# Kernel optimization log

Hardware: AMD Instinct MI355X
Metric: run time of the kernel (lower is better)

Reference implementation:

```python
import jax, jax.numpy as jnp
import numpy as np
from jax import lax

EPS = 1e-5
NUM_GROUPS = 32
OFFSET_SCALE = 1.0
K = 3            # deformable conv kernel size
KK = K * K
DWK = 7          # depthwise kernel size for offset predictor


def group_norm(x, gamma, beta, num_groups=NUM_GROUPS):
    B, C, H, W = x.shape
    xg = x.reshape(B, num_groups, C // num_groups, H, W)
    m = xg.mean(axis=(2, 3, 4), keepdims=True)
    v = xg.var(axis=(2, 3, 4), keepdims=True)
    xn = ((xg - m) * lax.rsqrt(v + EPS)).reshape(B, C, H, W)
    return xn * gamma[None, :, None, None] + beta[None, :, None, None]


def bilinear_gather(x, py, px):
    # x: [B,C,H,W]; py, px: [B,KK,H,W] absolute sample coords -> [B,C,KK,H,W]
    B, C, H, W = x.shape
    y0 = jnp.floor(py)
    x0 = jnp.floor(px)
    wy1 = py - y0
    wx1 = px - x0
    wy0 = 1.0 - wy1
    wx0 = 1.0 - wx1
    xf = x.reshape(B, C, H * W)

    def gather(yi, xi):
        valid = (yi >= 0) & (yi <= H - 1) & (xi >= 0) & (xi <= W - 1)
        yc = jnp.clip(yi, 0, H - 1).astype(jnp.int32)
        xc = jnp.clip(xi, 0, W - 1).astype(jnp.int32)
        idx = (yc * W + xc).reshape(B, -1)                      # [B, KK*H*W]
        g = jax.vmap(lambda a, i: a[:, i])(xf, idx)             # [B, C, KK*H*W]
        g = g.reshape(B, C, KK, H, W)
        return g * valid.astype(x.dtype)[:, None]

    out = (gather(y0, x0) * (wy0 * wx0)[:, None]
           + gather(y0, x0 + 1.0) * (wy0 * wx1)[:, None]
           + gather(y0 + 1.0, x0) * (wy1 * wx0)[:, None]
           + gather(y0 + 1.0, x0 + 1.0) * (wy1 * wx1)[:, None])
    return out


def deform_conv(x, dw, pw, pwb, w, b):
    # x: [B,C,H,W]; dw: [C,1,DWK,DWK] depthwise; pw: [2*KK,C,1,1]; w: [O,C,K,K]
    B, C, H, W = x.shape
    dn = ('NCHW', 'OIHW', 'NCHW')
    f = lax.conv_general_dilated(x, dw, (1, 1), 'SAME',
                                 feature_group_count=C, dimension_numbers=dn)
    off = lax.conv_general_dilated(f, pw, (1, 1), 'SAME', dimension_numbers=dn)
    off = (off + pwb[None, :, None, None]) * OFFSET_SCALE       # [B,2*KK,H,W]
    off = off.reshape(B, KK, 2, H, W)
    ks = jnp.arange(K, dtype=x.dtype) - (K - 1) / 2             # [-1,0,1]
    ky = jnp.repeat(ks, K)                                      # [KK]
    kx = jnp.tile(ks, K)
    yy, xx = jnp.meshgrid(jnp.arange(H, dtype=x.dtype),
                          jnp.arange(W, dtype=x.dtype), indexing='ij')
    py = yy[None, None] + ky[None, :, None, None] + off[:, :, 0]  # [B,KK,H,W]
    px = xx[None, None] + kx[None, :, None, None] + off[:, :, 1]
    sampled = bilinear_gather(x, py, px)                        # [B,C,KK,H,W]
    O = w.shape[0]
    out = jnp.einsum('bckhw,ock->bohw', sampled, w.reshape(O, C, KK))
    return out + b[None, :, None, None]


def setup_inputs() -> dict:
    key = jax.random.key(0)
    ks = jax.random.split(key, 10)
    B, C, H, W = 4, 256, 64, 64
    O = C
    x = jax.random.normal(ks[0], (B, C, H, W), dtype=jnp.float32)

    def conv_w(k, shape, fan_in):
        return jax.random.normal(k, shape, dtype=jnp.float32) / np.sqrt(fan_in)

    inp = {
        'x': x,
        'gn1_g': jnp.ones((C,), jnp.float32), 'gn1_b': jnp.zeros((C,), jnp.float32),
        'dw1': conv_w(ks[1], (C, 1, DWK, DWK), DWK * DWK),
        'pw1': jax.random.normal(ks[2], (2 * KK, C, 1, 1), jnp.float32) * 0.01,
        'pwb1': jnp.zeros((2 * KK,), jnp.float32),
        'w1': conv_w(ks[3], (O, C, K, K), C * KK),
        'b1': jnp.zeros((O,), jnp.float32),
        'gn2_g': jnp.ones((O,), jnp.float32), 'gn2_b': jnp.zeros((O,), jnp.float32),
        'dw2': conv_w(ks[4], (O, 1, DWK, DWK), DWK * DWK),
        'pw2': jax.random.normal(ks[5], (2 * KK, O, 1, 1), jnp.float32) * 0.01,
        'pwb2': jnp.zeros((2 * KK,), jnp.float32),
        'w2': conv_w(ks[6], (O, O, K, K), O * KK),
        'b2': jnp.zeros((O,), jnp.float32),
    }
    return inp


def reference(x, gn1_g, gn1_b, dw1, pw1, pwb1, w1, b1,
              gn2_g, gn2_b, dw2, pw2, pwb2, w2, b2):
    h = jax.nn.relu(group_norm(x, gn1_g, gn1_b))
    h = deform_conv(h, dw1, pw1, pwb1, w1, b1)
    h = jax.nn.relu(group_norm(h, gn2_g, gn2_b))
    # Dropout / DropPath are identity in eval mode
    h = deform_conv(h, dw2, pw2, pwb2, w2, b2)
    return h + x  # shortcut is Identity (in_channels == out_channels)
```

## Files before the change

### kernel.cpp

```cpp
#include <hip/hip_runtime.h>

#define B_    4
#define C_    256
#define H_    64
#define W_    64
#define HW_   4096
#define NG_   32
#define CPG_  8
#define KK_   9
#define NOFF_ 18

typedef __attribute__((ext_vector_type(8))) short short8;
typedef __attribute__((ext_vector_type(4))) short short4v;
typedef __attribute__((ext_vector_type(4))) float floatx4;
typedef __attribute__((ext_vector_type(16))) float floatx16;

static __device__ __forceinline__ short f2bf(float f) {
    union { float f; unsigned u; } v; v.f = f;
    unsigned r = v.u + 0x7fff + ((v.u >> 16) & 1);
    return (short)(r >> 16);
}
static __device__ __forceinline__ float bf2f(short s) {
    union { unsigned u; float f; } v;
    v.u = ((unsigned)(unsigned short)s) << 16;
    return v.f;
}
static __device__ __forceinline__ unsigned pkbf(float lo, float hi) {
    unsigned r;
    asm("v_cvt_pk_bf16_f32 %0, %1, %2" : "=v"(r) : "v"(lo), "v"(hi));
    return r;
}

__global__ __launch_bounds__(1024) void gn_relu_f32_kernel(
    const float* __restrict__ in, const float* __restrict__ gamma,
    const float* __restrict__ beta, short* __restrict__ outb)
{
    __shared__ float cache[32768];
    __shared__ float red[32];
    __shared__ float sh_rs, sh_m;
    int b = blockIdx.x >> 5;
    int g = blockIdx.x & 31;
    const int N = CPG_ * HW_;
    size_t base = ((size_t)(b * C_ + g * CPG_)) * HW_;
    const float4* in4 = (const float4*)(in + base);
    int t = threadIdx.x;

    float s = 0.f, ss = 0.f;
    for (int i = t; i < N / 4; i += 1024) {
        float4 v = in4[i];
        *(float4*)&cache[i * 4] = v;
        s  += v.x + v.y + v.z + v.w;
        ss += v.x * v.x + v.y * v.y + v.z * v.z + v.w * v.w;
    }
    #pragma unroll
    for (int off = 32; off > 0; off >>= 1) {
        s  += __shfl_down(s, off, 64);
        ss += __shfl_down(ss, off, 64);
    }
    int wid = t >> 6;
    if ((t & 63) == 0) { red[wid] = s; red[16 + wid] = ss; }
    __syncthreads();
    if (t == 0) {
        float S = 0.f, SS = 0.f;
        #pragma unroll
        for (int i = 0; i < 16; ++i) { S += red[i]; SS += red[16 + i]; }
        float m = S / (float)N;
        float var = SS / (float)N - m * m;
        sh_rs = rsqrtf(var + 1e-5f);
        sh_m = m;
    }
    __syncthreads();
    float rs = sh_rs, m = sh_m;
    short4v* out4 = (short4v*)(outb + base);
    for (int i = t; i < N / 4; i += 1024) {
        int ch = g * CPG_ + (i >> 10);
        float ga = gamma[ch] * rs;
        float be = beta[ch] - m * ga;
        float4 v = *(const float4*)&cache[i * 4];
        short4v o;
        o.x = f2bf(fmaxf(fmaf(v.x, ga, be), 0.f));
        o.y = f2bf(fmaxf(fmaf(v.y, ga, be), 0.f));
        o.z = f2bf(fmaxf(fmaf(v.z, ga, be), 0.f));
        o.w = f2bf(fmaxf(fmaf(v.w, ga, be), 0.f));
        out4[i] = o;
    }
}

__global__ __launch_bounds__(1024) void gn_apply_bf16_kernel(
    const short* __restrict__ in, const float* __restrict__ gstats,
    const float* __restrict__ gamma, const float* __restrict__ beta,
    short* __restrict__ outb)
{
    int blk = blockIdx.x;
    int b = blk >> 7, g = (blk >> 2) & 31, qq = blk & 3;
    const float Ninv = 1.f / (float)(CPG_ * HW_);
    int sidx = b * 32 + g;
    float m   = gstats[sidx] * Ninv;
    float var = gstats[128 + sidx] * Ninv - m * m;
    float rs  = rsqrtf(var + 1e-5f);
    size_t base = ((size_t)(b * C_ + g * CPG_)) * HW_;
    const short4v* in4 = (const short4v*)(in + base);
    short4v* out4 = (short4v*)(outb + base);
    int t = threadIdx.x;
    int i0 = qq * 2048;
    for (int i = i0 + t; i < i0 + 2048; i += 1024) {
        int ch = g * CPG_ + (i >> 10);
        float ga = gamma[ch] * rs;
        float be = beta[ch] - m * ga;
        short4v sv = in4[i];
        short4v o;
        o.x = f2bf(fmaxf(fmaf(bf2f(sv.x), ga, be), 0.f));
        o.y = f2bf(fmaxf(fmaf(bf2f(sv.y), ga, be), 0.f));
        o.z = f2bf(fmaxf(fmaf(bf2f(sv.z), ga, be), 0.f));
        o.w = f2bf(fmaxf(fmaf(bf2f(sv.w), ga, be), 0.f));
        out4[i] = o;
    }
}

__global__ __launch_bounds__(256) void dw7t_tr_kernel(
    const short* __restrict__ in,
    const float* __restrict__ dwk,
    short* __restrict__ fdwt,
    short* __restrict__ ht)
{
    __shared__ __align__(16) char smem[78112];
    int t = threadIdx.x;
    int blk = blockIdx.x;
    if (blk < 256) {
        short (*tile)[38][72] = (short(*)[38][72])smem;
        float (*wk8)[49]      = (float(*)[49])(smem + 43776);
        short (*outs)[2048]   = (short(*)[2048])(smem + 45344);
        int b = blk >> 6, o8 = (blk >> 1) & 31, rh = blk & 1;
        int c0 = o8 * 8;
        unsigned* tz = (unsigned*)smem;
        for (int i = t; i < 10944; i += 256) tz[i] = 0u;
        for (int i = t; i < 392; i += 256)
            wk8[i / 49][i % 49] = dwk[(c0 + i / 49) * 49 + (i % 49)];
        __syncthreads();
        for (int ch = 0; ch < 8; ++ch) {
            const short* src = in + ((size_t)(b * C_ + c0 + ch)) * HW_;
            for (int i = t; i < 608; i += 256) {
                int rr = i >> 4, xq = i & 15;
                int ry = rh * 32 + rr - 3;
                if (ry >= 0 && ry < 64) {
                    short4v v = *(const short4v*)(src + ry * 64 + xq * 4);
                    *(short4v*)&tile[ch][rr][4 + xq * 4] = v;
                }
            }
        }
        __syncthreads();
        for (int it = 0; it < 16; ++it) {
            int q = it * 256 + t;
            int ch = q >> 9, y = (q >> 4) & 31, x0 = (q & 15) << 2;
            float a0 = 0.f, a1 = 0.f, a2 = 0.f, a3 = 0.f;
            const float* wr0 = wk8[ch];
            #pragma unroll
            for (int dy = 0; dy < 7; ++dy) {
                const short* trw = &tile[ch][y + dy][x0];
                short4v s0 = *(const short4v*)trw;
                short4v s1 = *(const short4v*)(trw + 4);
                short4v s2 = *(const short4v*)(trw + 8);
                float r[12] = {bf2f(s0.x), bf2f(s0.y), bf2f(s0.z), bf2f(s0.w),
                               bf2f(s1.x), bf2f(s1.y), bf2f(s1.z), bf2f(s1.w),
                               bf2f(s2.x), bf2f(s2.y), bf2f(s2.z), bf2f(s2.w)};
                const float* wr = wr0 + dy * 7;
                #pragma unroll
                for (int dx = 0; dx < 7; ++dx) {
                    float wv = wr[dx];
                    a0 = fmaf(r[dx + 1], wv, a0);
                    a1 = fmaf(r[dx + 2], wv, a1);
                    a2 = fmaf(r[dx + 3], wv, a2);
                    a3 = fmaf(r[dx + 4], wv, a3);
                }
            }
            short4v o;
            o.x = f2bf(a0); o.y = f2bf(a1); o.z = f2bf(a2); o.w = f2bf(a3);
            *(short4v*)&outs[ch][y * 64 + x0] = o;
        }
        __syncthreads();
        for (int it = 0; it < 8; ++it) {
            int p = it * 256 + t;
            short8 v;
            #pragma unroll
            for (int ch = 0; ch < 8; ++ch) v[ch] = outs[ch][p];
            *(short8*)(fdwt + (((size_t)(b * 64 + rh * 32 + (p >> 6)) * 32 + o8) * 64
                               + (p & 63)) * 8) = v;
        }
    } else {
        unsigned* ltile = (unsigned*)smem;
        int q0 = blk - 256;
        int q = ((q0 & 7) << 5) | (q0 >> 3);
        int b = q >> 6;
        int px0 = (q & 63) * 64;
        const short* sb = in + (size_t)b * C_ * HW_;
        int pq4 = t & 15, cphi = t >> 4;
        #pragma unroll
        for (int i = 0; i < 8; ++i) {
            int cp = i * 16 + cphi;
            const short* r0 = sb + (size_t)(2 * cp) * HW_ + px0 + pq4 * 4;
            short4v lo = *(const short4v*)r0;
            short4v hi = *(const short4v*)(r0 + HW_);
            #pragma unroll
            for (int j = 0; j < 4; ++j) {
                int pl = pq4 * 4 + j;
                unsigned wrd = (unsigned)(unsigned short)lo[j]
                             | ((unsigned)(unsigned short)hi[j] << 16);
                ltile[pl * 132 + (cp ^ ((pl & 7) << 2))] = wrd;
            }
        }
        __syncthreads();
        int co = t & 31, ph2 = t >> 5;
        #pragma unroll
        for (int r = 0; r < 8; ++r) {
            int pl = r * 8 + ph2;
            uint4 v = *(const uint4*)&ltile[pl * 132 + ((co * 4) ^ ((pl & 7) << 2))];
            *(uint4*)(ht + ((size_t)b * HW_ + px0 + pl) * C_ + co * 8) = v;
        }
    }
}

__global__ __launch_bounds__(256) void wpack_all_kernel(
    const float* __restrict__ w1, const float* __restrict__ w2,
    const float* __restrict__ pw1, const float* __restrict__ pw2,
    short* __restrict__ wp1, short* __restrict__ wp2,
    short* __restrict__ ppk1, short* __restrict__ ppk2)
{
    int blk = blockIdx.x;
    if (blk < 4608) {
        const float* w = (blk < 2304) ? w1 : w2;
        short* wp = (blk < 2304) ? wp1 : wp2;
        int src = (blk % 2304) * 256 + threadIdx.x;
        float v = w[src];
        int o = src / (C_ * KK_);
        int r = src - o * (C_ * KK_);
        int c = r / KK_;
        int g = r - c * KK_;
        int ot   = o >> 5;
        int lane = (o & 31) | (((c >> 3) & 1) << 5);
        int j    = c & 7;
        int slab = g * 16 + (c >> 4);
        wp[(slab << 12) | (ot << 9) | (lane << 3) | j] = f2bf(v);
    } else {
        int q = blk - 4608;
        const float* pw = (q < 32) ? pw1 : pw2;
        short* ppk = (q < 32) ? ppk1 : ppk2;
        int idx = (q & 31) * 256 + threadIdx.x;
        int j = idx & 7, lane = (idx >> 3) & 63;
        int ot = (idx >> 9) & 1, sl = idx >> 10;
        int o = ot * 16 + (lane & 15);
        int k = sl * 32 + (lane >> 4) * 8 + j;
        ppk[idx] = (o < NOFF_) ? f2bf(pw[o * C_ + k]) : (short)0;
    }
}

__global__ __launch_bounds__(1024, 4) void deform_fused_kernel(
    const short* __restrict__ ht,   const short* __restrict__ fdw,
    const short* __restrict__ ppk,  const float* __restrict__ pwb,
    const short* __restrict__ wp,   const float* __restrict__ bias,
    const float* __restrict__ resid, float* __restrict__ outf,
    short* __restrict__ outb,       float* __restrict__ gstats)
{
    int lb = ((blockIdx.x & 7) << 5) | (blockIdx.x >> 3);
    int b = lb >> 6;
    int row = lb & 63;
    __shared__ int   i00[576], i01[576], i10[576], i11[576];
    __shared__ float c00[576], c01[576], c10[576], c11[576];
    __shared__ __align__(16) short sbuf[2][2][8192];
    __shared__ float stat_lds[16][8];
    float* off_lds = (float*)&sbuf[0][0][0];
    int t = threadIdx.x;
    int wv = t >> 6, lane = t & 63;
    int pq = lane >> 4, pr = lane & 15;
    int l31 = lane & 31, hi = lane >> 5;

    if (wv < 8) {
        int ot = wv & 1, ptw = wv >> 1;
        int px = ptw * 16 + pr;
        const short8* fdw8 = (const short8*)fdw;
        size_t fbase = ((size_t)(b * 64 + row)) * 32;
        const short8* ap = (const short8*)ppk;
        floatx4 pacc = (floatx4){0.f, 0.f, 0.f, 0.f};
        #pragma unroll
        for (int sl = 0; sl < 8; ++sl) {
            short8 af = ap[(sl * 2 + ot) * 64 + lane];
            short8 bf = fdw8[(fbase + sl * 4 + pq) * 64 + px];
            pacc = __builtin_amdgcn_mfma_f32_16x16x32_bf16(af, bf, pacc, 0, 0, 0);
        }
        #pragma unroll
        for (int r = 0; r < 4; ++r) {
            int o = ot * 16 + pq * 4 + r;
            if (o < NOFF_) off_lds[o * 64 + px] = pacc[r] + pwb[o];
        }
    }
    __syncthreads();

    if (t < 576) {
        int e = t;
        int k = e >> 6, p = e & 63;
        float offy = off_lds[(2 * k) * 64 + p];
        float offx = off_lds[(2 * k + 1) * 64 + p];
        float py = (float)row + (float)(k / 3 - 1) + offy;
        float px = (float)p   + (float)(k % 3 - 1) + offx;
        float y0f = floorf(py), x0f = floorf(px);
        float wy1 = py - y0f, wx1 = px - x0f;
        float wy0 = 1.f - wy1, wx0 = 1.f - wx1;
        float y1f = y0f + 1.f, x1f = x0f + 1.f;
        bool vy0 = (y0f >= 0.f) && (y0f <= 63.f);
        bool vy1 = (y1f >= 0.f) && (y1f <= 63.f);
        bool vx0 = (x0f >= 0.f) && (x0f <= 63.f);
        bool vx1 = (x1f >= 0.f) && (x1f <= 63.f);
        int iy0 = (int)fminf(fmaxf(y0f, 0.f), 63.f);
        int iy1 = (int)fminf(fmaxf(y1f, 0.f), 63.f);
        int ix0 = (int)fminf(fmaxf(x0f, 0.f), 63.f);
        int ix1 = (int)fminf(fmaxf(x1f, 0.f), 63.f);
        i00[e] = iy0 * 64 + ix0; i01[e] = iy0 * 64 + ix1;
        i10[e] = iy1 * 64 + ix0; i11[e] = iy1 * 64 + ix1;
        c00[e] = (vy0 && vx0) ? wy0 * wx0 : 0.f;
        c01[e] = (vy0 && vx1) ? wy0 * wx1 : 0.f;
        c10[e] = (vy1 && vx0) ? wy1 * wx0 : 0.f;
        c11[e] = (vy1 && vx1) ? wy1 * wx1 : 0.f;
    }
    __syncthreads();

    int c8a = t & 7;
    int pan = (t >> 3) & 1;
    int spx = t >> 4;
    const short* hb0 = ht + ((size_t)b * HW_) * C_ + pan * 128 + c8a * 8;
    const short* hb1 = hb0 + 64;
    int slotA = (c8a ^ (spx & 15)) * 8;
    int slotB = ((c8a + 8) ^ (spx & 15)) * 8;
    int srow = spx * 128;

    short8 ra[4], rb[4];
    auto prefetch = [&](int g) {
        int e = g * 64 + spx;
        int a00 = i00[e], a01 = i01[e], a10 = i10[e], a11 = i11[e];
        ra[0] = *(const short8*)(hb0 + (size_t)a00 * C_);
        ra[1] = *(const short8*)(hb0 + (size_t)a01 * C_);
        ra[2] = *(const short8*)(hb0 + (size_t)a10 * C_);
        ra[3] = *(const short8*)(hb0 + (size_t)a11 * C_);
        rb[0] = *(const short8*)(hb1 + (size_t)a00 * C_);
        rb[1] = *(const short8*)(hb1 + (size_t)a01 * C_);
        rb[2] = *(const short8*)(hb1 + (size_t)a10 * C_);
        rb[3] = *(const short8*)(hb1 + (size_t)a11 * C_);
    };
    auto stage_write = [&](int g, int bi) {
        int e = g * 64 + spx;
        float w00 = c00[e], w01 = c01[e], w10 = c10[e], w11 = c11[e];
        uint4 va, vb;
        float f0, f1;
        #define BLEND(R, J) (w00 * bf2f(R[0][J]) + w01 * bf2f(R[1][J]) \
                           + w10 * bf2f(R[2][J]) + w11 * bf2f(R[3][J]))
        f0 = BLEND(ra, 0); f1 = BLEND(ra, 1); va.x = pkbf(f0, f1);
        f0 = BLEND(ra, 2); f1 = BLEND(ra, 3); va.y = pkbf(f0, f1);
        f0 = BLEND(ra, 4); f1 = BLEND(ra, 5); va.z = pkbf(f0, f1);
        f0 = BLEND(ra, 6); f1 = BLEND(ra, 7); va.w = pkbf(f0, f1);
        f0 = BLEND(rb, 0); f1 = BLEND(rb, 1); vb.x = pkbf(f0, f1);
        f0 = BLEND(rb, 2); f1 = BLEND(rb, 3); vb.y = pkbf(f0, f1);
        f0 = BLEND(rb, 4); f1 = BLEND(rb, 5); vb.z = pkbf(f0, f1);
        f0 = BLEND(rb, 6); f1 = BLEND(rb, 7); vb.w = pkbf(f0, f1);
        #undef BLEND
        short* sp = &sbuf[bi][pan][srow];
        *(uint4*)&sp[slotA] = va;
        *(uint4*)&sp[slotB] = vb;
    };

    int pairId = wv & 7;
    int half = wv >> 3;

    floatx16 acc[2];
    #pragma unroll
    for (int i = 0; i < 16; ++i) { acc[0][i] = 0.f; acc[1][i] = 0.f; }

    prefetch(0);
    stage_write(0, 0);
    prefetch(1);
    __syncthreads();

    const short8* wp8 = (const short8*)wp;
    int msk = l31 & 15;

    for (int g = 0; g < 9; ++g) {
        const short* sb = &sbuf[g & 1][half][0];
        #pragma unroll
        for (int q4 = 0; q4 < 2; ++q4) {
            short8 af[4];
            #pragma unroll
            for (int qq = 0; qq < 4; ++qq)
                af[qq] = wp8[(size_t)(((g * 16 + half * 8 + q4 * 4 + qq) * 8 + pairId) * 64 + lane)];
            #pragma unroll
            for (int qq = 0; qq < 4; ++qq) {
                int ksl = q4 * 4 + qq;
                int so = ((((ksl << 1) | hi) ^ msk) << 3);
                short8 b0 = *(const short8*)&sb[l31 * 128 + so];
                short8 b1 = *(const short8*)&sb[(32 + l31) * 128 + so];
                acc[0] = __builtin_amdgcn_mfma_f32_32x32x16_bf16(af[qq], b0, acc[0], 0, 0, 0);
                acc[1] = __builtin_amdgcn_mfma_f32_32x32x16_bf16(af[qq], b1, acc[1], 0, 0, 0);
            }
        }
        if (g + 1 < 9) {
            stage_write(g + 1, (g + 1) & 1);
            if (g + 2 < 9) prefetch(g + 2);
        }
        __syncthreads();
    }

    float* xch = (float*)&sbuf[0][0][0];
    int wreg = (pairId * 2 + half) * 1024;
    floatx16 aw = half ? acc[0] : acc[1];
    floatx4* xq = (floatx4*)xch;
    #pragma unroll
    for (int j = 0; j < 4; ++j) {
        floatx4 v = {aw[j * 4 + 0], aw[j * 4 + 1], aw[j * 4 + 2], aw[j * 4 + 3]};
        xq[(wreg >> 2) + j * 64 + lane] = v;
    }
    __syncthreads();
    int rreg = (pairId * 2 + (half ^ 1)) * 1024;
    floatx16 ac = half ? acc[1] : acc[0];
    #pragma unroll
    for (int j = 0; j < 4; ++j) {
        floatx4 v = xq[(rreg >> 2) + j * 64 + lane];
        ac[j * 4 + 0] += v.x; ac[j * 4 + 1] += v.y;
        ac[j * 4 + 2] += v.z; ac[j * 4 + 3] += v.w;
    }

    float sj[4] = {0.f, 0.f, 0.f, 0.f};
    float qj[4] = {0.f, 0.f, 0.f, 0.f};
    #pragma unroll
    for (int r = 0; r < 16; ++r) {
        int o = pairId * 32 + (r & 3) + 8 * (r >> 2) + 4 * hi;
        float v = ac[r] + bias[o];
        size_t ob = ((size_t)(b * C_ + o)) * HW_ + row * 64 + half * 32 + l31;
        if (outf) {
            if (resid) v += resid[ob];
            outf[ob] = v;
        } else {
            outb[ob] = f2bf(v);
            sj[r >> 2] += v;
            qj[r >> 2] += v * v;
        }
    }
    if (gstats) {
        #pragma unroll
        for (int off = 32; off > 0; off >>= 1) {
            #pragma unroll
            for (int j = 0; j < 4; ++j) {
                sj[j] += __shfl_down(sj[j], off, 64);
                qj[j] += __shfl_down(qj[j], off, 64);
            }
        }
        if (lane == 0) {
            #pragma unroll
            for (int j = 0; j < 4; ++j) {
                stat_lds[wv][j] = sj[j];
                stat_lds[wv][4 + j] = qj[j];
            }
        }
        __syncthreads();
        if (t < 32) {
            int pid = t >> 2, j = t & 3;
            float sT = stat_lds[pid][j] + stat_lds[pid + 8][j];
            float qT = stat_lds[pid][4 + j] + stat_lds[pid + 8][4 + j];
            int idx = b * 32 + pid * 4 + j;
            atomicAdd(&gstats[idx], sT);
            atomicAdd(&gstats[128 + idx], qT);
        }
    }
}

extern "C" void kernel_launch(void* const* d_in, const int* in_sizes, int n_in,
                              void* d_out, int out_size, void* d_ws, size_t ws_size,
                              hipStream_t stream)
{
    const float* x     = (const float*)d_in[0];
    const float* gn1_g = (const float*)d_in[1];
    const float* gn1_b = (const float*)d_in[2];
    const float* dw1   = (const float*)d_in[3];
    const float* pw1   = (const float*)d_in[4];
    const float* pwb1  = (const float*)d_in[5];
    const float* w1    = (const float*)d_in[6];
    const float* b1    = (const float*)d_in[7];
    const float* gn2_g = (const float*)d_in[8];
    const float* gn2_b = (const float*)d_in[9];
    const float* dw2   = (const float*)d_in[10];
    const float* pw2   = (const float*)d_in[11];
    const float* pwb2  = (const float*)d_in[12];
    const float* w2    = (const float*)d_in[13];
    const float* b2    = (const float*)d_in[14];
    float* out = (float*)d_out;

    float* ws   = (float*)d_ws;
    short* y1b  = (short*)ws;
    short* hbf  = (short*)(ws + 2097152);
    short* hbt  = (short*)(ws + 4194304);
    short* fdwt = (short*)(ws + 8388608);
    short* wp1  = (short*)(ws + 10485760);
    short* wp2  = (short*)(ws + 10780672);
    short* ppk1 = (short*)(ws + 11075584);
    short* ppk2 = (short*)(ws + 11079680);
    float* gstats = ws + 11083776;

    wpack_all_kernel<<<4672, 256, 0, stream>>>(w1, w2, pw1, pw2,
                                               wp1, wp2, ppk1, ppk2);
    hipMemsetAsync(gstats, 0, 256 * sizeof(float), stream);

    gn_relu_f32_kernel<<<B_ * NG_, 1024, 0, stream>>>(x, gn1_g, gn1_b, hbf);
    dw7t_tr_kernel<<<512, 256, 0, stream>>>(hbf, dw1, fdwt, hbt);
    deform_fused_kernel<<<B_ * H_, 1024, 0, stream>>>(
        hbt, fdwt, ppk1, pwb1, wp1, b1, nullptr, nullptr, y1b, gstats);

    gn_apply_bf16_kernel<<<512, 1024, 0, stream>>>(y1b, gstats, gn2_g, gn2_b, hbf);
    dw7t_tr_kernel<<<512, 256, 0, stream>>>(hbf, dw2, fdwt, hbt);
    deform_fused_kernel<<<B_ * H_, 1024, 0, stream>>>(
        hbt, fdwt, ppk2, pwb2, wp2, b2, x, out, nullptr, nullptr);
}
```

Before: 242.8 us.

## Fuse second GroupNorm apply into depthwise/transpose kernel with per-row partial stats

```diff
diff --git a/kernel.cpp b/kernel.cpp
--- a/kernel.cpp
+++ b/kernel.cpp
@@ -86,64 +86,65 @@
     }
 }
 
-__global__ __launch_bounds__(1024) void gn_apply_bf16_kernel(
-    const short* __restrict__ in, const float* __restrict__ gstats,
-    const float* __restrict__ gamma, const float* __restrict__ beta,
-    short* __restrict__ outb)
-{
-    int blk = blockIdx.x;
-    int b = blk >> 7, g = (blk >> 2) & 31, qq = blk & 3;
-    const float Ninv = 1.f / (float)(CPG_ * HW_);
-    int sidx = b * 32 + g;
-    float m   = gstats[sidx] * Ninv;
-    float var = gstats[128 + sidx] * Ninv - m * m;
-    float rs  = rsqrtf(var + 1e-5f);
-    size_t base = ((size_t)(b * C_ + g * CPG_)) * HW_;
-    const short4v* in4 = (const short4v*)(in + base);
-    short4v* out4 = (short4v*)(outb + base);
-    int t = threadIdx.x;
-    int i0 = qq * 2048;
-    for (int i = i0 + t; i < i0 + 2048; i += 1024) {
-        int ch = g * CPG_ + (i >> 10);
-        float ga = gamma[ch] * rs;
-        float be = beta[ch] - m * ga;
-        short4v sv = in4[i];
-        short4v o;
-        o.x = f2bf(fmaxf(fmaf(bf2f(sv.x), ga, be), 0.f));
-        o.y = f2bf(fmaxf(fmaf(bf2f(sv.y), ga, be), 0.f));
-        o.z = f2bf(fmaxf(fmaf(bf2f(sv.z), ga, be), 0.f));
-        o.w = f2bf(fmaxf(fmaf(bf2f(sv.w), ga, be), 0.f));
-        out4[i] = o;
-    }
-}
-
 __global__ __launch_bounds__(256) void dw7t_tr_kernel(
     const short* __restrict__ in,
     const float* __restrict__ dwk,
     short* __restrict__ fdwt,
-    short* __restrict__ ht)
+    short* __restrict__ ht,
+    const float* __restrict__ pstats,
+    const float* __restrict__ gamma, const float* __restrict__ beta)
 {
-    __shared__ __align__(16) char smem[78112];
+    __shared__ __align__(16) char smem[78144];
+    const float Ninv = 1.f / (float)(CPG_ * HW_);
     int t = threadIdx.x;
     int blk = blockIdx.x;
     if (blk < 256) {
         short (*tile)[38][72] = (short(*)[38][72])smem;
         float (*wk8)[49]      = (float(*)[49])(smem + 43776);
         short (*outs)[2048]   = (short(*)[2048])(smem + 45344);
+        float* gsh            = (float*)(smem + 78112);
         int b = blk >> 6, o8 = (blk >> 1) & 31, rh = blk & 1;
         int c0 = o8 * 8;
+        if (pstats && t < 64) {
+            const float* pp = pstats + (((size_t)(b * 64 + t)) * 32 + o8) * 2;
+            float s = pp[0], q = pp[1];
+            #pragma unroll
+            for (int off = 32; off > 0; off >>= 1) {
+                s += __shfl_down(s, off, 64);
+                q += __shfl_down(q, off, 64);
+            }
+            if (t == 0) {
+                float m = s * Ninv;
+                float var = q * Ninv - m * m;
+                gsh[0] = m;
+                gsh[1] = rsqrtf(var + 1e-5f);
+            }
+        }
         unsigned* tz = (unsigned*)smem;
         for (int i = t; i < 10944; i += 256) tz[i] = 0u;
         for (int i = t; i < 392; i += 256)
             wk8[i / 49][i % 49] = dwk[(c0 + i / 49) * 49 + (i % 49)];
         __syncthreads();
+        float m_g = 0.f, rs_g = 0.f;
+        if (pstats) { m_g = gsh[0]; rs_g = gsh[1]; }
         for (int ch = 0; ch < 8; ++ch) {
             const short* src = in + ((size_t)(b * C_ + c0 + ch)) * HW_;
+            float ga = 0.f, be = 0.f;
+            if (pstats) {
+                ga = gamma[c0 + ch] * rs_g;
+                be = beta[c0 + ch] - m_g * ga;
+            }
             for (int i = t; i < 608; i += 256) {
                 int rr = i >> 4, xq = i & 15;
                 int ry = rh * 32 + rr - 3;
                 if (ry >= 0 && ry < 64) {
                     short4v v = *(const short4v*)(src + ry * 64 + xq * 4);
+                    if (pstats) {
+                        v.x = f2bf(fmaxf(fmaf(bf2f(v.x), ga, be), 0.f));
+                        v.y = f2bf(fmaxf(fmaf(bf2f(v.y), ga, be), 0.f));
+                        v.z = f2bf(fmaxf(fmaf(bf2f(v.z), ga, be), 0.f));
+                        v.w = f2bf(fmaxf(fmaf(bf2f(v.w), ga, be), 0.f));
+                    }
                     *(short4v*)&tile[ch][rr][4 + xq * 4] = v;
                 }
             }
@@ -188,11 +189,30 @@
         }
     } else {
         unsigned* ltile = (unsigned*)smem;
+        float* gmrs = (float*)(smem + 65536);
         int q0 = blk - 256;
         int q = ((q0 & 7) << 5) | (q0 >> 3);
         int b = q >> 6;
         int px0 = (q & 63) * 64;
         const short* sb = in + (size_t)b * C_ * HW_;
+        if (pstats) {
+            int gq = t >> 3, rq = t & 7;
+            float s = 0.f, qs = 0.f;
+            for (int rr = rq; rr < 64; rr += 8) {
+                const float* pp = pstats + (((size_t)(b * 64 + rr)) * 32 + gq) * 2;
+                s += pp[0]; qs += pp[1];
+            }
+            s  += __shfl_down(s, 4, 64);  qs += __shfl_down(qs, 4, 64);
+            s  += __shfl_down(s, 2, 64);  qs += __shfl_down(qs, 2, 64);
+            s  += __shfl_down(s, 1, 64);  qs += __shfl_down(qs, 1, 64);
+            if (rq == 0) {
+                float m = s * Ninv;
+                float var = qs * Ninv - m * m;
+                gmrs[gq] = m;
+                gmrs[32 + gq] = rsqrtf(var + 1e-5f);
+            }
+        }
+        __syncthreads();
         int pq4 = t & 15, cphi = t >> 4;
         #pragma unroll
         for (int i = 0; i < 8; ++i) {
@@ -200,11 +220,25 @@
             const short* r0 = sb + (size_t)(2 * cp) * HW_ + px0 + pq4 * 4;
             short4v lo = *(const short4v*)r0;
             short4v hi = *(const short4v*)(r0 + HW_);
+            float ga0 = 0.f, be0 = 0.f, ga1 = 0.f, be1 = 0.f;
+            if (pstats) {
+                int g0 = cp >> 2;
+                float mm = gmrs[g0], rr2 = gmrs[32 + g0];
+                ga0 = gamma[2 * cp] * rr2;     be0 = beta[2 * cp] - mm * ga0;
+                ga1 = gamma[2 * cp + 1] * rr2; be1 = beta[2 * cp + 1] - mm * ga1;
+            }
             #pragma unroll
             for (int j = 0; j < 4; ++j) {
                 int pl = pq4 * 4 + j;
-                unsigned wrd = (unsigned)(unsigned short)lo[j]
-                             | ((unsigned)(unsigned short)hi[j] << 16);
+                unsigned wrd;
+                if (pstats) {
+                    float v0 = fmaxf(fmaf(bf2f(lo[j]), ga0, be0), 0.f);
+                    float v1 = fmaxf(fmaf(bf2f(hi[j]), ga1, be1), 0.f);
+                    wrd = pkbf(v0, v1);
+                } else {
+                    wrd = (unsigned)(unsigned short)lo[j]
+                        | ((unsigned)(unsigned short)hi[j] << 16);
+                }
                 ltile[pl * 132 + (cp ^ ((pl & 7) << 2))] = wrd;
             }
         }
@@ -258,7 +292,7 @@
     const short* __restrict__ ppk,  const float* __restrict__ pwb,
     const short* __restrict__ wp,   const float* __restrict__ bias,
     const float* __restrict__ resid, float* __restrict__ outf,
-    short* __restrict__ outb,       float* __restrict__ gstats)
+    short* __restrict__ outb,       float* __restrict__ pstats)
 {
     int lb = ((blockIdx.x & 7) << 5) | (blockIdx.x >> 3);
     int b = lb >> 6;
@@ -440,7 +474,7 @@
             qj[r >> 2] += v * v;
         }
     }
-    if (gstats) {
+    if (pstats) {
         #pragma unroll
         for (int off = 32; off > 0; off >>= 1) {
             #pragma unroll
@@ -461,9 +495,9 @@
             int pid = t >> 2, j = t & 3;
             float sT = stat_lds[pid][j] + stat_lds[pid + 8][j];
             float qT = stat_lds[pid][4 + j] + stat_lds[pid + 8][4 + j];
-            int idx = b * 32 + pid * 4 + j;
-            atomicAdd(&gstats[idx], sT);
-            atomicAdd(&gstats[128 + idx], qT);
+            float* pp = pstats + (((size_t)(b * 64 + row)) * 32 + pid * 4 + j) * 2;
+            pp[0] = sT;
+            pp[1] = qT;
         }
     }
 }
@@ -498,19 +532,19 @@
     short* wp2  = (short*)(ws + 10780672);
     short* ppk1 = (short*)(ws + 11075584);
     short* ppk2 = (short*)(ws + 11079680);
-    float* gstats = ws + 11083776;
+    float* pstats = ws + 11083776;
 
     wpack_all_kernel<<<4672, 256, 0, stream>>>(w1, w2, pw1, pw2,
                                                wp1, wp2, ppk1, ppk2);
-    hipMemsetAsync(gstats, 0, 256 * sizeof(float), stream);
 
     gn_relu_f32_kernel<<<B_ * NG_, 1024, 0, stream>>>(x, gn1_g, gn1_b, hbf);
-    dw7t_tr_kernel<<<512, 256, 0, stream>>>(hbf, dw1, fdwt, hbt);
+    dw7t_tr_kernel<<<512, 256, 0, stream>>>(hbf, dw1, fdwt, hbt,
+                                            nullptr, nullptr, nullptr);
     deform_fused_kernel<<<B_ * H_, 1024, 0, stream>>>(
-        hbt, fdwt, ppk1, pwb1, wp1, b1, nullptr, nullptr, y1b, gstats);
-
-    gn_apply_bf16_kernel<<<512, 1024, 0, stream>>>(y1b, gstats, gn2_g, gn2_b, hbf);
-    dw7t_tr_kernel<<<512, 256, 0, stream>>>(hbf, dw2, fdwt, hbt);
+        hbt, fdwt, ppk1, pwb1, wp1, b1, nullptr, nullptr, y1b, pstats);
+
+    dw7t_tr_kernel<<<512, 256, 0, stream>>>(y1b, dw2, fdwt, hbt,
+                                            pstats, gn2_g, gn2_b);
     deform_fused_kernel<<<B_ * H_, 1024, 0, stream>>>(
         hbt, fdwt, ppk2, pwb2, wp2, b2, x, out, nullptr, nullptr);
 }
```

Result: faster. 236.4 us, median of 2 (-2.6%).
